# Kernel optimization log

Hardware: AMD Instinct MI355X
Metric: run time of the kernel (lower is better)

The kernel has to match this reference:

```python
import jax, jax.numpy as jnp
import numpy as np

S, B, C = 14, 2, 20          # grid size, boxes per cell, classes
LAMBDA_COORD, LAMBDA_NOOBJ = 5.0, 0.5
NCH = 5 * B + C              # 30 channels


def setup_inputs() -> dict:
    key = jax.random.key(0)
    k1, k2, k3 = jax.random.split(key, 3)
    Nb = 4096
    # positive values: loss takes sqrt(w), sqrt(h)
    pred = jax.random.uniform(k1, (Nb, S, S, NCH), dtype=jnp.float32, minval=0.05, maxval=1.0)
    target = jax.random.uniform(k2, (Nb, S, S, NCH), dtype=jnp.float32, minval=0.05, maxval=1.0)
    # binarize conf channels so coord (conf>0) / noobj (conf==0) partition the cells
    objf = (jax.random.uniform(k3, (Nb, S, S)) < 0.3).astype(jnp.float32)
    for b in range(B):
        target = target.at[..., 4 + 5 * b].set(objf)
    return {"pred_tensor": pred, "target_tensor": target}


def _to_xyxy(box):
    # box [..., 5] (or [..., B, 5]): cell-relative x,y and global w,h -> corners
    xy = box[..., :2] / S
    half = 0.5 * box[..., 2:4]
    return jnp.concatenate([xy - half, xy + half], axis=-1)


def reference(pred_tensor, target_tensor):
    pred, target = pred_tensor, target_tensor
    obj = (target[..., 4] > 0).astype(pred.dtype)      # [Nb,S,S]
    noobj = (target[..., 4] == 0).astype(pred.dtype)   # [Nb,S,S]

    pb = pred[..., :5 * B].reshape(pred.shape[:3] + (B, 5))     # [Nb,S,S,B,5]
    tb = target[..., :5 * B].reshape(target.shape[:3] + (B, 5))  # [Nb,S,S,B,5]

    # no-object confidence loss: conf channel of every box slot in noobj cells
    loss_noobj = jnp.sum(noobj[..., None] * (pb[..., 4] - tb[..., 4]) ** 2)

    # IoU of each of B predicted boxes vs the (first) target box of the cell
    pxy = _to_xyxy(pb)                        # [Nb,S,S,B,4]
    txy = _to_xyxy(tb[..., 0, :])[..., None, :]  # [Nb,S,S,1,4]
    lt = jnp.maximum(pxy[..., :2], txy[..., :2])
    rb = jnp.minimum(pxy[..., 2:], txy[..., 2:])
    wh = jnp.clip(rb - lt, 0.0)
    inter = wh[..., 0] * wh[..., 1]           # [Nb,S,S,B]
    area_p = (pxy[..., 2] - pxy[..., 0]) * (pxy[..., 3] - pxy[..., 1])
    area_t = (txy[..., 2] - txy[..., 0]) * (txy[..., 3] - txy[..., 1])
    iou = inter / (area_p + area_t - inter)

    max_iou = jax.lax.stop_gradient(jnp.max(iou, axis=-1))  # torch uses .data (detach)
    r = jnp.argmax(iou, axis=-1)              # responsible box index [Nb,S,S]

    pr = jnp.take_along_axis(pb, r[..., None, None], axis=3)[..., 0, :]  # [Nb,S,S,5]
    tr = jnp.take_along_axis(tb, r[..., None, None], axis=3)[..., 0, :]

    m = obj
    loss_xy = jnp.sum(m[..., None] * (pr[..., :2] - tr[..., :2]) ** 2)
    # guard sqrt in masked-out cells (values there don't matter)
    safe_pwh = jnp.where(m[..., None] > 0, pr[..., 2:4], 1.0)
    safe_twh = jnp.where(m[..., None] > 0, tr[..., 2:4], 1.0)
    loss_wh = jnp.sum(m[..., None] * (jnp.sqrt(safe_pwh) - jnp.sqrt(safe_twh)) ** 2)
    loss_obj = jnp.sum(m * (pr[..., 4] - max_iou) ** 2)
    loss_class = jnp.sum(m[..., None] * (pred[..., 5 * B:] - target[..., 5 * B:]) ** 2)

    loss = LAMBDA_COORD * (loss_xy + loss_wh) + loss_obj + LAMBDA_NOOBJ * loss_noobj + loss_class
    return loss / pred.shape[0]
```

## Files before the change

### kernel.cpp

```cpp
#include <hip/hip_runtime.h>


#define S_GRID 14
#define NB 4096
#define NCELL (NB * S_GRID * S_GRID)
#define NCH 30
#define CELLS_PER_BLOCK 256
#define NBLOCKS (NCELL / CELLS_PER_BLOCK)
#define FLOATS_PER_BLOCK (CELLS_PER_BLOCK * NCH)

#define GLOBAL_AS __attribute__((address_space(1)))
#define LDS_AS    __attribute__((address_space(3)))

__device__ __forceinline__ void async_copy16(const float* g, float* l) {
    __builtin_amdgcn_global_load_lds((const GLOBAL_AS void*)g, (LDS_AS void*)l,
                                     16, 0, 0);
}

__global__ __launch_bounds__(256) void yolo_loss_partial(
    const float* __restrict__ pred, const float* __restrict__ target,
    float* __restrict__ partial)
{
    __shared__ float ps[FLOATS_PER_BLOCK];
    __shared__ float ts[FLOATS_PER_BLOCK];

    const int tid = threadIdx.x;
    const size_t base = (size_t)blockIdx.x * FLOATS_PER_BLOCK;

#pragma unroll
    for (int r = 0; r < 8; ++r) {
        int idx = r * 256 + tid;
        if (idx < FLOATS_PER_BLOCK / 4) {
            async_copy16(pred + base + (size_t)idx * 4, ps + idx * 4);
            async_copy16(target + base + (size_t)idx * 4, ts + idx * 4);
        }
    }
    __syncthreads();

    float loss;
    {
        float p[NCH], t[NCH];
        const float2* p2 = (const float2*)(ps + tid * NCH);
        const float2* t2 = (const float2*)(ts + tid * NCH);
#pragma unroll
        for (int i = 0; i < NCH / 2; ++i) {
            float2 a = p2[i]; p[2 * i] = a.x; p[2 * i + 1] = a.y;
            float2 b = t2[i]; t[2 * i] = b.x; t[2 * i + 1] = b.y;
        }

        const float t4 = t[4];
        const bool obj = (t4 > 0.0f);

        float dn0 = p[4] - t[4];
        float dn1 = p[9] - t[9];
        float noobj_l = (t4 == 0.0f) ? (dn0 * dn0 + dn1 * dn1) : 0.0f;

        const float invS = 1.0f / 14.0f;
        float tcx = t[0] * invS, tcy = t[1] * invS;
        float tx1 = tcx - 0.5f * t[2], ty1 = tcy - 0.5f * t[3];
        float tx2 = tcx + 0.5f * t[2], ty2 = tcy + 0.5f * t[3];
        float area_t = (tx2 - tx1) * (ty2 - ty1);

        float iou[2];
#pragma unroll
        for (int b = 0; b < 2; ++b) {
            const float* pb = p + 5 * b;
            float cx = pb[0] * invS, cy = pb[1] * invS;
            float x1 = cx - 0.5f * pb[2], y1 = cy - 0.5f * pb[3];
            float x2 = cx + 0.5f * pb[2], y2 = cy + 0.5f * pb[3];
            float lx = fmaxf(x1, tx1), ly = fmaxf(y1, ty1);
            float rx = fminf(x2, tx2), ry = fminf(y2, ty2);
            float wx = fmaxf(rx - lx, 0.0f), wy = fmaxf(ry - ly, 0.0f);
            float inter = wx * wy;
            float area_p = (x2 - x1) * (y2 - y1);
            iou[b] = inter / (area_p + area_t - inter);
        }

        int r = (iou[1] > iou[0]) ? 1 : 0;
        float max_iou = fmaxf(iou[0], iou[1]);

        float obj_l = 0.0f;
        if (obj) {
            const float* pr = p + 5 * r;
            const float* tr = t + 5 * r;
            float dx = pr[0] - tr[0], dy = pr[1] - tr[1];
            float lxy = dx * dx + dy * dy;
            float dw = sqrtf(pr[2]) - sqrtf(tr[2]);
            float dh = sqrtf(pr[3]) - sqrtf(tr[3]);
            float lwh = dw * dw + dh * dh;
            float dob = pr[4] - max_iou;
            float lob = dob * dob;
            float lcls = 0.0f;
#pragma unroll
            for (int c = 10; c < 30; ++c) {
                float d = p[c] - t[c];
                lcls += d * d;
            }
            obj_l = 5.0f * (lxy + lwh) + lob + lcls;
        }
        loss = obj_l + 0.5f * noobj_l;
    }

    float v = loss;
#pragma unroll
    for (int off = 32; off > 0; off >>= 1)
        v += __shfl_down(v, off, 64);

    __shared__ float red[4];
    const int lane = threadIdx.x & 63;
    const int wid = threadIdx.x >> 6;
    if (lane == 0) red[wid] = v;
    __syncthreads();
    if (threadIdx.x == 0)
        partial[blockIdx.x] = red[0] + red[1] + red[2] + red[3];
}

__global__ __launch_bounds__(256) void yolo_loss_finalize(
    const float* __restrict__ partial, float* __restrict__ out)
{
    double s = 0.0;
    for (int i = threadIdx.x; i < NBLOCKS; i += 256)
        s += (double)partial[i];

    __shared__ double sh[256];
    sh[threadIdx.x] = s;
    __syncthreads();
#pragma unroll
    for (int step = 128; step > 0; step >>= 1) {
        if (threadIdx.x < step) sh[threadIdx.x] += sh[threadIdx.x + step];
        __syncthreads();
    }
    if (threadIdx.x == 0)
        out[0] = (float)(sh[0] / (double)NB);
}

extern "C" void kernel_launch(void* const* d_in, const int* in_sizes, int n_in,
                              void* d_out, int out_size, void* d_ws, size_t ws_size,
                              hipStream_t stream) {
    const float* pred = (const float*)d_in[0];
    const float* target = (const float*)d_in[1];
    float* out = (float*)d_out;
    float* partial = (float*)d_ws;

    yolo_loss_partial<<<NBLOCKS, 256, 0, stream>>>(pred, target, partial);
    yolo_loss_finalize<<<1, 256, 0, stream>>>(partial, out);
}
```

Before: 206.5 us.

## Use per-wave LDS tiles reused for pred then target, drop block sync

Each wave now loads its own 64-cell tile into a private LDS slice and waits with s_waitcnt instead of a block barrier. The slice first holds pred and is then reused for target, which halves LDS per block. The class loss is computed while streaming target values, so fewer registers are live. Per-wave partials replace the block-level reduction. The goal is higher occupancy (launch bounds now request 5 blocks) and less barrier stalling, at the cost of serialising the two loads within each wave and a finalize that sums four times as many partials.

Result: slower. 214.3 us (+3.8%).

```diff
diff --git a/kernel.cpp b/kernel.cpp
--- a/kernel.cpp
+++ b/kernel.cpp
@@ -1,53 +1,76 @@
 #include <hip/hip_runtime.h>
 
 
-#define S_GRID 14
 #define NB 4096
-#define NCELL (NB * S_GRID * S_GRID)
-#define NCH 30
-#define CELLS_PER_BLOCK 256
-#define NBLOCKS (NCELL / CELLS_PER_BLOCK)
-#define FLOATS_PER_BLOCK (CELLS_PER_BLOCK * NCH)
+#define NCELL (NB * 14 * 14)
+#define CELLS_PER_WAVE 64
+#define NTILES (NCELL / CELLS_PER_WAVE)
+#define WAVES_PER_BLOCK 4
+#define NBLOCKS (NTILES / WAVES_PER_BLOCK)
+#define TILE_FLOATS (CELLS_PER_WAVE * 30)
 
 #define GLOBAL_AS __attribute__((address_space(1)))
 #define LDS_AS    __attribute__((address_space(3)))
 
-__device__ __forceinline__ void async_copy16(const float* g, float* l) {
+__device__ __forceinline__ void async16(const float* g, float* l) {
     __builtin_amdgcn_global_load_lds((const GLOBAL_AS void*)g, (LDS_AS void*)l,
                                      16, 0, 0);
 }
 
-__global__ __launch_bounds__(256) void yolo_loss_partial(
+__global__ __launch_bounds__(256, 5) void yolo_partial(
     const float* __restrict__ pred, const float* __restrict__ target,
     float* __restrict__ partial)
 {
-    __shared__ float ps[FLOATS_PER_BLOCK];
-    __shared__ float ts[FLOATS_PER_BLOCK];
+    __shared__ float buf[WAVES_PER_BLOCK][TILE_FLOATS];
 
-    const int tid = threadIdx.x;
-    const size_t base = (size_t)blockIdx.x * FLOATS_PER_BLOCK;
+    const int lane = threadIdx.x & 63;
+    const int wid  = threadIdx.x >> 6;
+    const int tile = blockIdx.x * WAVES_PER_BLOCK + wid;
+    float* wbuf = buf[wid];
+    const size_t base = (size_t)tile * TILE_FLOATS;
 
 #pragma unroll
-    for (int r = 0; r < 8; ++r) {
-        int idx = r * 256 + tid;
-        if (idx < FLOATS_PER_BLOCK / 4) {
-            async_copy16(pred + base + (size_t)idx * 4, ps + idx * 4);
-            async_copy16(target + base + (size_t)idx * 4, ts + idx * 4);
+    for (int r = 0; r < 7; ++r)
+        async16(pred + base + (size_t)(r * 64 + lane) * 4, wbuf + (r * 64 + lane) * 4);
+    if (lane < 32)
+        async16(pred + base + (size_t)(448 + lane) * 4, wbuf + (448 + lane) * 4);
+    __asm volatile("s_waitcnt vmcnt(0)" ::: "memory");
+
+    float p[30];
+    {
+        const float2* s2 = (const float2*)(wbuf + lane * 30);
+#pragma unroll
+        for (int i = 0; i < 15; ++i) {
+            float2 a = s2[i]; p[2 * i] = a.x; p[2 * i + 1] = a.y;
         }
     }
-    __syncthreads();
+    __asm volatile("s_waitcnt lgkmcnt(0)" ::: "memory");
+
+#pragma unroll
+    for (int r = 0; r < 7; ++r)
+        async16(target + base + (size_t)(r * 64 + lane) * 4, wbuf + (r * 64 + lane) * 4);
+    if (lane < 32)
+        async16(target + base + (size_t)(448 + lane) * 4, wbuf + (448 + lane) * 4);
+    __asm volatile("s_waitcnt vmcnt(0)" ::: "memory");
+
+    float t[10];
+    float cls = 0.0f;
+    {
+        const float2* s2 = (const float2*)(wbuf + lane * 30);
+#pragma unroll
+        for (int i = 0; i < 5; ++i) {
+            float2 a = s2[i]; t[2 * i] = a.x; t[2 * i + 1] = a.y;
+        }
+#pragma unroll
+        for (int i = 5; i < 15; ++i) {
+            float2 a = s2[i];
+            float d0 = p[2 * i] - a.x, d1 = p[2 * i + 1] - a.y;
+            cls += d0 * d0 + d1 * d1;
+        }
+    }
 
     float loss;
     {
-        float p[NCH], t[NCH];
-        const float2* p2 = (const float2*)(ps + tid * NCH);
-        const float2* t2 = (const float2*)(ts + tid * NCH);
-#pragma unroll
-        for (int i = 0; i < NCH / 2; ++i) {
-            float2 a = p2[i]; p[2 * i] = a.x; p[2 * i + 1] = a.y;
-            float2 b = t2[i]; t[2 * i] = b.x; t[2 * i + 1] = b.y;
-        }
-
         const float t4 = t[4];
         const bool obj = (t4 > 0.0f);
 
@@ -90,13 +113,7 @@
             float lwh = dw * dw + dh * dh;
             float dob = pr[4] - max_iou;
             float lob = dob * dob;
-            float lcls = 0.0f;
-#pragma unroll
-            for (int c = 10; c < 30; ++c) {
-                float d = p[c] - t[c];
-                lcls += d * d;
-            }
-            obj_l = 5.0f * (lxy + lwh) + lob + lcls;
+            obj_l = 5.0f * (lxy + lwh) + lob + cls;
         }
         loss = obj_l + 0.5f * noobj_l;
     }
@@ -105,21 +122,15 @@
 #pragma unroll
     for (int off = 32; off > 0; off >>= 1)
         v += __shfl_down(v, off, 64);
-
-    __shared__ float red[4];
-    const int lane = threadIdx.x & 63;
-    const int wid = threadIdx.x >> 6;
-    if (lane == 0) red[wid] = v;
-    __syncthreads();
-    if (threadIdx.x == 0)
-        partial[blockIdx.x] = red[0] + red[1] + red[2] + red[3];
+    if (lane == 0)
+        partial[tile] = v;
 }
 
-__global__ __launch_bounds__(256) void yolo_loss_finalize(
+__global__ __launch_bounds__(256) void yolo_finalize(
     const float* __restrict__ partial, float* __restrict__ out)
 {
     double s = 0.0;
-    for (int i = threadIdx.x; i < NBLOCKS; i += 256)
+    for (int i = threadIdx.x; i < NTILES; i += 256)
         s += (double)partial[i];
 
     __shared__ double sh[256];
@@ -142,6 +153,6 @@
     float* out = (float*)d_out;
     float* partial = (float*)d_ws;
 
-    yolo_loss_partial<<<NBLOCKS, 256, 0, stream>>>(pred, target, partial);
-    yolo_loss_finalize<<<1, 256, 0, stream>>>(partial, out);
+    yolo_partial<<<NBLOCKS, 256, 0, stream>>>(pred, target, partial);
+    yolo_finalize<<<1, 256, 0, stream>>>(partial, out);
 }
```
